# Kernel optimization log

Hardware: AMD Instinct MI355X
Metric: run time of the kernel (lower is better)

The kernel has to match this reference:

```python
import jax, jax.numpy as jnp
import numpy as np

HEADS = 8
HEAD_DIM = 48  # 384 / 8
WINDOW = 64
SCALE = HEAD_DIM ** -0.5


def setup_inputs() -> dict:
    key = jax.random.key(0)
    ks = jax.random.split(key, 8)
    B, T, C, M = 128, 256, 384, 512
    x = jax.random.normal(ks[0], (B, T, C), dtype=jnp.float32)
    mem = jax.random.normal(ks[1], (M, C), dtype=jnp.float32)
    loss_mask = jax.random.uniform(ks[2], (B, T), dtype=jnp.float32)
    # parameters (torch Linear equivalents, stored as [in, out])
    s = 1.0 / np.sqrt(C)
    Wqkv = jax.random.uniform(ks[3], (C, 3 * C), dtype=jnp.float32, minval=-s, maxval=s)
    bqkv = jax.random.uniform(ks[4], (3 * C,), dtype=jnp.float32, minval=-s, maxval=s)
    Wproj = jax.random.uniform(ks[5], (C, C), dtype=jnp.float32, minval=-s, maxval=s)
    bproj = jax.random.uniform(ks[6], (C,), dtype=jnp.float32, minval=-s, maxval=s)
    gate = jnp.ones((C,), dtype=jnp.float32)
    return {"x": x, "mem": mem, "loss_mask": loss_mask, "Wqkv": Wqkv,
            "bqkv": bqkv, "Wproj": Wproj, "bproj": bproj, "gate": gate}


def reference(x, mem, loss_mask, Wqkv, bqkv, Wproj, bproj, gate):
    B, T, C = x.shape
    M = mem.shape[0]
    qkv = x @ Wqkv + bqkv                       # [B, T, 3C]
    q, k, v = jnp.split(qkv, 3, axis=-1)
    # concat raw memory onto keys/values
    m = jnp.broadcast_to(mem[None], (B, M, C))
    k = jnp.concatenate([m, k], axis=1)          # [B, M+T, C]
    v = jnp.concatenate([m, v], axis=1)

    def heads(t):
        return t.reshape(B, -1, HEADS, HEAD_DIM).transpose(0, 2, 1, 3)
    qh, kh, vh = heads(q), heads(k), heads(v)    # [B, H, L, hd]

    att = jnp.einsum('bhqd,bhkd->bhqk', qh, kh) * SCALE  # [B, H, T, M+T]
    # causal + local-window mask on the self (non-mem) key block; mem unmasked
    i = jnp.arange(T)[:, None]
    j = jnp.arange(T)[None, :]
    self_mask = (j <= i) & (jnp.abs(i - j) <= WINDOW)    # [T, T]
    full_mask = jnp.concatenate(
        [jnp.ones((T, M), dtype=bool), self_mask], axis=1)  # [T, M+T]
    att = jnp.where(full_mask[None, None], att, -jnp.inf)
    p = jax.nn.softmax(att, axis=-1)
    y = jnp.einsum('bhqk,bhkd->bhqd', p, vh)     # [B, H, T, hd]
    y = y.transpose(0, 2, 1, 3).reshape(B, T, C)
    out = (y * gate) @ Wproj + bproj
    out = out * loss_mask[..., None]
    return out
```

## Files before the change

### kernel.cpp

```cpp
#include <hip/hip_runtime.h>
#include <hip/hip_bf16.h>

typedef __bf16 bf16_t;
typedef __bf16 bf16x4 __attribute__((ext_vector_type(4)));
typedef __bf16 bf16x8 __attribute__((ext_vector_type(8)));
typedef float f32x4 __attribute__((ext_vector_type(4)));
typedef unsigned int u32;
typedef unsigned int u32x4 __attribute__((ext_vector_type(4)));

struct alignas(16) V16 { unsigned long long x, y; };

#define SC2 0.20823437553929245f
#define NEGBIG -3.0e38f

static __device__ __forceinline__ bf16_t f2b(float f) {
  union { float f; unsigned u; } v; v.f = f;
  unsigned r = v.u + 0x7fffu + ((v.u >> 16) & 1u);
  unsigned short h = (unsigned short)(r >> 16);
  return __builtin_bit_cast(bf16_t, h);
}

static __device__ __forceinline__ f32x4 mfma16(bf16x8 a, bf16x8 b, f32x4 c) {
  return __builtin_amdgcn_mfma_f32_16x16x32_bf16(a, b, c, 0, 0, 0);
}

static __device__ __forceinline__ float exp2f_(float x) {
#if __has_builtin(__builtin_amdgcn_exp2f)
  return __builtin_amdgcn_exp2f(x);
#else
  return __expf(x * 0.6931471805599453f);
#endif
}

static __device__ __forceinline__ u32 cvtpk(float lo, float hi) {
  u32 r;
  asm("v_cvt_pk_bf16_f32 %0, %1, %2" : "=v"(r) : "v"(lo), "v"(hi));
  return r;
}

static __device__ __forceinline__ void gload16(const void* g, void* l) {
  __builtin_amdgcn_global_load_lds(
      (__attribute__((address_space(1))) void*)(unsigned long long)(size_t)g,
      (__attribute__((address_space(3))) void*)(unsigned)(size_t)l,
      16, 0, 0);
}

__global__ void k_xconv(const float* __restrict__ x, bf16_t* __restrict__ xb) {
  size_t i = ((size_t)blockIdx.x * 256 + threadIdx.x) * 8;
  float4 a0 = *(const float4*)(x + i);
  float4 a1 = *(const float4*)(x + i + 4);
  bf16x8 t;
  t[0] = f2b(a0.x); t[1] = f2b(a0.y); t[2] = f2b(a0.z); t[3] = f2b(a0.w);
  t[4] = f2b(a1.x); t[5] = f2b(a1.y); t[6] = f2b(a1.z); t[7] = f2b(a1.w);
  *(bf16x8*)(xb + i) = t;
}

__global__ void k_wprep(const float* __restrict__ W, bf16_t* __restrict__ Wp) {
  int idx = blockIdx.x * 256 + threadIdx.x;
  if (idx >= 1536 * 384) return;
  int c2 = idx / 384, k = idx - c2 * 384;
  int sec = c2 >> 9, within = c2 & 511, hh = within >> 6, d = within & 63;
  float v = (d < 48) ? W[k * 1152 + sec * 384 + hh * 48 + d] : 0.f;
  Wp[idx] = f2b(v);
}

__global__ void k_bprep(const float* __restrict__ bq, float* __restrict__ bp) {
  int c2 = blockIdx.x * 256 + threadIdx.x;
  if (c2 >= 1536) return;
  int sec = c2 >> 9, within = c2 & 511, hh = within >> 6, d = within & 63;
  bp[c2] = (d < 48) ? bq[sec * 384 + hh * 48 + d] : 0.f;
}

template<int K, int N>
__global__ void k_convT(const float* __restrict__ W, bf16_t* __restrict__ Wt) {
  int idx = blockIdx.x * 256 + threadIdx.x;
  if (idx >= K * N) return;
  int n = idx / K, k = idx - n * K;
  Wt[idx] = f2b(W[k * N + n]);
}

__global__ void k_memh(const float* __restrict__ mem, bf16_t* __restrict__ memh) {
  int idx = blockIdx.x * 256 + threadIdx.x;
  int h = idx >> 15;
  int m = (idx >> 6) & 511;
  int d = idx & 63;
  float v = (d < 48) ? mem[m * 384 + h * 48 + d] : 0.f;
  memh[idx] = f2b(v);
}

__global__ void k_memT(const float* __restrict__ mem, bf16_t* __restrict__ memT) {
  int idx = blockIdx.x * 256 + threadIdx.x;
  int h = idx / (48 * 512);
  int r = idx - h * 48 * 512;
  int d = r >> 9;
  int m = r & 511;
  memT[idx] = f2b(mem[m * 384 + h * 48 + d]);
}

__global__ __launch_bounds__(256) void k_gemm_qkv(
    const bf16_t* __restrict__ xb, const bf16_t* __restrict__ Wt,
    const float* __restrict__ biasp,
    bf16_t* __restrict__ qh, bf16_t* __restrict__ kh, bf16_t* __restrict__ vT)
{
  __shared__ __align__(16) char smem[32768];
  const int tid = threadIdx.x;
  const int lane = tid & 63;
  const int j16 = lane & 15;
  const int g = lane >> 4;
  const int wid = tid >> 6;
  const int wr = wid >> 1, wc = wid & 1;
  const int rowBase = blockIdx.x * 128;
  const int colBase = blockIdx.y * 128;
  const int srow = tid >> 2, skc = (tid & 3) * 8;

  f32x4 acc[4][4] = {};

#define STAGE_G(k0, bufidx) do { \
    char* A_ = smem + (bufidx) * 16384; \
    char* B_ = A_ + 8192; \
    gload16(xb + (size_t)(rowBase + srow) * 384 + (k0) + skc, A_ + tid * 16); \
    gload16(xb + (size_t)(rowBase + 64 + srow) * 384 + (k0) + skc, A_ + 4096 + tid * 16); \
    gload16(Wt + (size_t)(colBase + srow) * 384 + (k0) + skc, B_ + tid * 16); \
    gload16(Wt + (size_t)(colBase + 64 + srow) * 384 + (k0) + skc, B_ + 4096 + tid * 16); \
  } while (0)

  STAGE_G(0, 0);
  __syncthreads();
  for (int i = 0; i < 12; ++i) {
    const int cur = i & 1;
    if (i < 11) STAGE_G((i + 1) * 32, cur ^ 1);
    const bf16_t* As = (const bf16_t*)(smem + cur * 16384);
    const bf16_t* Bs = As + 4096;
    bf16x8 af[4], bfr[4];
#pragma unroll
    for (int mb = 0; mb < 4; ++mb)
      af[mb] = *(const bf16x8*)&As[(wr * 64 + mb * 16 + j16) * 32 + g * 8];
#pragma unroll
    for (int nb = 0; nb < 4; ++nb)
      bfr[nb] = *(const bf16x8*)&Bs[(wc * 64 + nb * 16 + j16) * 32 + g * 8];
#pragma unroll
    for (int mb = 0; mb < 4; ++mb)
#pragma unroll
      for (int nb = 0; nb < 4; ++nb)
        acc[mb][nb] = mfma16(af[mb], bfr[nb], acc[mb][nb]);
    __syncthreads();
  }
#undef STAGE_G

  const int sec = colBase >> 9;
  const int b = rowBase >> 8;
  const int tBase = rowBase & 255;
  if (sec < 2) {
    bf16_t* dst0 = (sec == 0) ? qh : kh;
    const int hBase = (colBase - sec * 512) >> 6;
    bf16_t* C = (bf16_t*)smem;
#pragma unroll
    for (int nb = 0; nb < 4; ++nb) {
      const int c_loc = wc * 64 + nb * 16 + j16;
      const float bv = biasp[colBase + c_loc];
#pragma unroll
      for (int mb = 0; mb < 4; ++mb)
#pragma unroll
        for (int r = 0; r < 4; ++r) {
          const int t_loc = wr * 64 + mb * 16 + g * 4 + r;
          C[t_loc * 128 + c_loc] = f2b(acc[mb][nb][r] + bv);
        }
    }
    __syncthreads();
#pragma unroll
    for (int ch = 0; ch < 2; ++ch) {
      const int h = hBase + ch;
      bf16_t* dst = dst0 + (((size_t)(b * 8 + h) * 256 + tBase) << 6);
#pragma unroll
      for (int p = 0; p < 4; ++p) {
        const int k = tid + p * 256;
        const int t_loc = k >> 3;
        V16 v = *(const V16*)&C[t_loc * 128 + ch * 64 + (k & 7) * 8];
        *(V16*)&dst[(size_t)k * 8] = v;
      }
    }
  } else {
#pragma unroll
    for (int nb = 0; nb < 4; ++nb) {
      const int cl = wc * 64 + nb * 16 + j16;
      const int vcol = (colBase - 1024) + cl;
      const int hh = vcol >> 6, d = vcol & 63;
      const float bv = biasp[colBase + cl];
      if (d < 48) {
#pragma unroll
        for (int mb = 0; mb < 4; ++mb) {
          bf16x4 pk;
#pragma unroll
          for (int r = 0; r < 4; ++r) pk[r] = f2b(acc[mb][nb][r] + bv);
          const int t0 = tBase + wr * 64 + mb * 16 + g * 4;
          *(bf16x4*)&vT[((size_t)(b * 8 + hh) * 48 + d) * 256 + t0] = pk;
        }
      }
    }
  }
}

__global__ __launch_bounds__(512, 2) void k_attn(
    const bf16_t* __restrict__ qh, const bf16_t* __restrict__ kh,
    const bf16_t* __restrict__ vT, const bf16_t* __restrict__ memh,
    const bf16_t* __restrict__ memT,
    const float* __restrict__ gate, bf16_t* __restrict__ yp)
{
  __shared__ __align__(16) char smem[57344];
  const int tid = threadIdx.x;
  const int lane = tid & 63;
  const int j16 = lane & 15;
  const int g = lane >> 4;
  const int w = tid >> 6;
  const int qc = blockIdx.x, h = blockIdx.y, b = blockIdx.z;
  const int bh = b * 8 + h;
  const int qw = qc * 128 + w * 16;

  const int key1 = tid >> 3;
  const int doffK = (((tid & 7) << 4) ^ ((key1 & 7) << 4)) >> 1;
  const int dv1 = tid >> 4;
  const int kvV = (((tid & 15) << 4) ^ ((dv1 & 7) << 4)) >> 1;

  bf16x8 qf0, qf1;
  {
    const bf16_t* qp = qh + ((size_t)(bh << 8) + qw + j16) * 64 + g * 8;
    qf0 = *(const bf16x8*)qp;
    qf1 = *(const bf16x8*)(qp + 32);
  }
  float m_r = -1e30f, l_r = 0.f;
  f32x4 o0 = {}, o1 = {}, o2 = {};
  const int nt = (qc == 1) ? 6 : 5;

#define STAGE_A(it_, buf_) do { \
    const bool im_ = (it_) < 4; \
    const int kb_ = im_ ? 0 : ((it_) - 4) * 128; \
    const bf16_t* ks_ = im_ ? memh + ((size_t)h * 512 + (it_) * 128) * 64 \
                            : kh + ((size_t)(bh << 8) + kb_) * 64; \
    const bf16_t* vs_; int vst_, vc_; \
    if (im_) { vs_ = memT + (size_t)h * 48 * 512; vst_ = 512; vc_ = (it_) * 128; } \
    else     { vs_ = vT + (size_t)bh * 48 * 256;  vst_ = 256; vc_ = kb_; } \
    char* K_ = smem + (buf_) * 28672; \
    char* V_ = K_ + 16384; \
    gload16(ks_ + key1 * 64 + doffK,        K_ + tid * 16); \
    gload16(ks_ + (key1 + 64) * 64 + doffK, K_ + 8192 + tid * 16); \
    gload16(vs_ + (size_t)dv1 * vst_ + vc_ + kvV, V_ + tid * 16); \
    if (tid < 256) \
      gload16(vs_ + (size_t)(dv1 + 32) * vst_ + vc_ + kvV, V_ + 8192 + tid * 16); \
  } while (0)

  STAGE_A(0, 0);
  __syncthreads();

  for (int it = 0; it < nt; ++it) {
    const int cur = it & 1;
    if (it + 1 < nt) STAGE_A(it + 1, cur ^ 1);

    const bool isMem = (it < 4);
    const int kb0 = (it - 4) * 128;
    if (isMem || !(kb0 > qw + 15 || kb0 + 127 < qw - 64)) {
      const char* K = smem + cur * 28672;
      const char* V = K + 16384;

      f32x4 s[8];
#pragma unroll
      for (int kb = 0; kb < 8; ++kb) {
        const int key = kb * 16 + j16;
        const int swz = (key & 7) << 4;
        bf16x8 k0v = *(const bf16x8*)(K + ((key * 128 + g * 16) ^ swz));
        bf16x8 k1v = *(const bf16x8*)(K + ((key * 128 + 64 + g * 16) ^ swz));
        f32x4 t4 = {};
        t4 = mfma16(k0v, qf0, t4);
        t4 = mfma16(k1v, qf1, t4);
        s[kb] = t4;
      }

      float mt = NEGBIG;
      if (!isMem) {
#pragma unroll
        for (int kb = 0; kb < 8; ++kb) {
          const int dbase = kb0 + kb * 16 + g * 4 - qw - j16;
#pragma unroll
          for (int r = 0; r < 4; ++r) {
            float sv = s[kb][r] * SC2;
            sv = ((unsigned)(dbase + r + 64) <= 64u) ? sv : NEGBIG;
            s[kb][r] = sv;
            mt = fmaxf(mt, sv);
          }
        }
      } else {
#pragma unroll
        for (int kb = 0; kb < 8; ++kb)
#pragma unroll
          for (int r = 0; r < 4; ++r) {
            float sv = s[kb][r] * SC2;
            s[kb][r] = sv;
            mt = fmaxf(mt, sv);
          }
      }
      mt = fmaxf(mt, __shfl_xor(mt, 16));
      mt = fmaxf(mt, __shfl_xor(mt, 32));

      const float mn = fmaxf(m_r, mt);
      const float alpha = exp2f_(m_r - mn);
      m_r = mn;
      o0 *= alpha; o1 *= alpha; o2 *= alpha;

      float ls = 0.f;
#pragma unroll
      for (int kb = 0; kb < 8; ++kb)
#pragma unroll
        for (int r = 0; r < 4; ++r) {
          float p = exp2f_(s[kb][r] - mn);
          s[kb][r] = p;
          ls += p;
        }
      ls += __shfl_xor(ls, 16);
      ls += __shfl_xor(ls, 32);
      l_r = l_r * alpha + ls;

      u32 pku[16];
#pragma unroll
      for (int kb = 0; kb < 8; ++kb) {
        pku[kb * 2]     = cvtpk(s[kb][0], s[kb][1]);
        pku[kb * 2 + 1] = cvtpk(s[kb][2], s[kb][3]);
      }

#pragma unroll
      for (int kqq = 0; kqq < 4; ++kqq) {
        u32x4 pv = { pku[4 * kqq], pku[4 * kqq + 1], pku[4 * kqq + 2], pku[4 * kqq + 3] };
        bf16x8 pb = __builtin_bit_cast(bf16x8, pv);
#pragma unroll
        for (int db = 0; db < 3; ++db) {
          const int d = db * 16 + j16;
          const int swzd = (d & 7) << 4;
          bf16x4 lo = *(const bf16x4*)(V + ((d * 256 + kqq * 64 + g * 8) ^ swzd));
          bf16x4 hi = *(const bf16x4*)(V + ((d * 256 + kqq * 64 + 32 + g * 8) ^ swzd));
          bf16x8 av = __builtin_shufflevector(lo, hi, 0, 1, 2, 3, 4, 5, 6, 7);
          if (db == 0)      o0 = mfma16(av, pb, o0);
          else if (db == 1) o1 = mfma16(av, pb, o1);
          else              o2 = mfma16(av, pb, o2);
        }
      }
    }
    __syncthreads();
  }
#undef STAGE_A

  const float inv = 1.0f / l_r;
  const int q = qw + j16;
#pragma unroll
  for (int db = 0; db < 3; ++db) {
    f32x4 oo = (db == 0) ? o0 : ((db == 1) ? o1 : o2);
    const int c0 = db * 16 + g * 4;
    bf16x4 pack;
#pragma unroll
    for (int r = 0; r < 4; ++r)
      pack[r] = f2b(oo[r] * inv * gate[h * 48 + c0 + r]);
    *(bf16x4*)(yp + ((size_t)(bh << 8) + q) * 48 + c0) = pack;
  }
}

__global__ __launch_bounds__(256) void k_gemm_proj(
    const bf16_t* __restrict__ yp, const bf16_t* __restrict__ Wt,
    const float* __restrict__ bias, const float* __restrict__ lm,
    float* __restrict__ out)
{
  __shared__ __align__(16) char smem[32768];
  const int tid = threadIdx.x;
  const int lane = tid & 63;
  const int j16 = lane & 15;
  const int g = lane >> 4;
  const int wid = tid >> 6;
  const int wr = wid >> 1, wc = wid & 1;
  const int rowBase = blockIdx.x * 128;
  const int colBase = blockIdx.y * 128;
  const int srow = tid >> 2, skc = (tid & 3) * 8;
  const int bb = rowBase >> 8, tb = rowBase & 255;

  f32x4 acc[4][4] = {};

#define STAGE_P(k0, bufidx) do { \
    char* A_ = smem + (bufidx) * 16384; \
    char* B_ = A_ + 8192; \
    const int c_ = (k0) + skc; \
    const int hh_ = (int)(((unsigned)c_ * 1366u) >> 16); \
    const int d_ = c_ - hh_ * 48; \
    gload16(yp + ((size_t)(bb * 8 + hh_) * 256 + tb + srow) * 48 + d_, A_ + tid * 16); \
    gload16(yp + ((size_t)(bb * 8 + hh_) * 256 + tb + 64 + srow) * 48 + d_, A_ + 4096 + tid * 16); \
    gload16(Wt + (size_t)(colBase + srow) * 384 + (k0) + skc, B_ + tid * 16); \
    gload16(Wt + (size_t)(colBase + 64 + srow) * 384 + (k0) + skc, B_ + 4096 + tid * 16); \
  } while (0)

  STAGE_P(0, 0);
  __syncthreads();
  for (int i = 0; i < 12; ++i) {
    const int cur = i & 1;
    if (i < 11) STAGE_P((i + 1) * 32, cur ^ 1);
    const bf16_t* As = (const bf16_t*)(smem + cur * 16384);
    const bf16_t* Bs = As + 4096;
    bf16x8 af[4], bfr[4];
#pragma unroll
    for (int mb = 0; mb < 4; ++mb)
      af[mb] = *(const bf16x8*)&As[(wr * 64 + mb * 16 + j16) * 32 + g * 8];
#pragma unroll
    for (int nb = 0; nb < 4; ++nb)
      bfr[nb] = *(const bf16x8*)&Bs[(wc * 64 + nb * 16 + j16) * 32 + g * 8];
#pragma unroll
    for (int mb = 0; mb < 4; ++mb)
#pragma unroll
      for (int nb = 0; nb < 4; ++nb)
        acc[mb][nb] = mfma16(af[mb], bfr[nb], acc[mb][nb]);
    __syncthreads();
  }
#undef STAGE_P

#pragma unroll
  for (int nb = 0; nb < 4; ++nb) {
    int col = colBase + wc * 64 + nb * 16 + j16;
    float bv = bias[col];
#pragma unroll
    for (int mb = 0; mb < 4; ++mb) {
#pragma unroll
      for (int r = 0; r < 4; ++r) {
        int row = rowBase + wr * 64 + mb * 16 + g * 4 + r;
        out[(size_t)row * 384 + col] = (acc[mb][nb][r] + bv) * lm[row];
      }
    }
  }
}

extern "C" void kernel_launch(void* const* d_in, const int* in_sizes, int n_in,
                              void* d_out, int out_size, void* d_ws, size_t ws_size,
                              hipStream_t stream) {
  const float* x     = (const float*)d_in[0];
  const float* mem   = (const float*)d_in[1];
  const float* lm    = (const float*)d_in[2];
  const float* Wqkv  = (const float*)d_in[3];
  const float* bqkv  = (const float*)d_in[4];
  const float* Wproj = (const float*)d_in[5];
  const float* bproj = (const float*)d_in[6];
  const float* gate  = (const float*)d_in[7];
  float* out = (float*)d_out;

  char* ws = (char*)d_ws;
  bf16_t* wqkvt = (bf16_t*)ws;  ws += (size_t)1536 * 384 * 2;
  float*  biasp = (float*)ws;   ws += (size_t)1536 * 4;
  bf16_t* wprojt = (bf16_t*)ws; ws += (size_t)384 * 384 * 2;
  bf16_t* memh = (bf16_t*)ws;   ws += (size_t)8 * 512 * 64 * 2;
  bf16_t* memT = (bf16_t*)ws;   ws += (size_t)8 * 48 * 512 * 2;
  bf16_t* qh = (bf16_t*)ws;     ws += (size_t)128 * 8 * 256 * 64 * 2;
  bf16_t* kh = (bf16_t*)ws;     ws += (size_t)128 * 8 * 256 * 64 * 2;
  bf16_t* vT = (bf16_t*)ws;     ws += (size_t)128 * 8 * 48 * 256 * 2;
  bf16_t* xb = (bf16_t*)ws;
  bf16_t* yp = xb;

  k_xconv<<<6144, 256, 0, stream>>>(x, xb);
  k_wprep<<<2304, 256, 0, stream>>>(Wqkv, wqkvt);
  k_bprep<<<6, 256, 0, stream>>>(bqkv, biasp);
  k_convT<384, 384><<<576, 256, 0, stream>>>(Wproj, wprojt);
  k_memh<<<1024, 256, 0, stream>>>(mem, memh);
  k_memT<<<768, 256, 0, stream>>>(mem, memT);
  k_gemm_qkv<<<dim3(256, 12), 256, 0, stream>>>(xb, wqkvt, biasp, qh, kh, vT);
  k_attn<<<dim3(2, 8, 128), 512, 0, stream>>>(qh, kh, vT, memh, memT, gate, yp);
  k_gemm_proj<<<dim3(256, 3), 256, 0, stream>>>(yp, wprojt, bproj, lm, out);
}
```

Measured before the change: 309.3 us.

## Unpad QKV GEMM, fuse prep kernels, merge query chunks in attention block

Combines all weight/memory preparation and q/k padding zeroing into one kernel, removes the padded 64-wide head layout from the QKV weight GEMM so it computes only 1152 columns, and folds the softmax scale into q. The attention kernel now processes both 128-query chunks per (batch, head) in one block, reusing each staged K/V tile for two query groups. This cuts GEMM work, launches and redundant K/V loads, at the cost of fewer attention blocks and higher register pressure.

```diff
diff --git a/kernel.cpp b/kernel.cpp
--- a/kernel.cpp
+++ b/kernel.cpp
@@ -55,51 +55,41 @@
   *(bf16x8*)(xb + i) = t;
 }
 
-__global__ void k_wprep(const float* __restrict__ W, bf16_t* __restrict__ Wp) {
+__global__ void k_prep(const float* __restrict__ Wqkv, const float* __restrict__ Wproj,
+                       const float* __restrict__ mem,
+                       bf16_t* __restrict__ wqkvt, bf16_t* __restrict__ wprojt,
+                       bf16_t* __restrict__ memh, bf16_t* __restrict__ memT,
+                       bf16_t* __restrict__ qh, bf16_t* __restrict__ kh) {
   int idx = blockIdx.x * 256 + threadIdx.x;
-  if (idx >= 1536 * 384) return;
-  int c2 = idx / 384, k = idx - c2 * 384;
-  int sec = c2 >> 9, within = c2 & 511, hh = within >> 6, d = within & 63;
-  float v = (d < 48) ? W[k * 1152 + sec * 384 + hh * 48 + d] : 0.f;
-  Wp[idx] = f2b(v);
-}
-
-__global__ void k_bprep(const float* __restrict__ bq, float* __restrict__ bp) {
-  int c2 = blockIdx.x * 256 + threadIdx.x;
-  if (c2 >= 1536) return;
-  int sec = c2 >> 9, within = c2 & 511, hh = within >> 6, d = within & 63;
-  bp[c2] = (d < 48) ? bq[sec * 384 + hh * 48 + d] : 0.f;
-}
-
-template<int K, int N>
-__global__ void k_convT(const float* __restrict__ W, bf16_t* __restrict__ Wt) {
-  int idx = blockIdx.x * 256 + threadIdx.x;
-  if (idx >= K * N) return;
-  int n = idx / K, k = idx - n * K;
-  Wt[idx] = f2b(W[k * N + n]);
-}
-
-__global__ void k_memh(const float* __restrict__ mem, bf16_t* __restrict__ memh) {
-  int idx = blockIdx.x * 256 + threadIdx.x;
-  int h = idx >> 15;
-  int m = (idx >> 6) & 511;
-  int d = idx & 63;
-  float v = (d < 48) ? mem[m * 384 + h * 48 + d] : 0.f;
-  memh[idx] = f2b(v);
-}
-
-__global__ void k_memT(const float* __restrict__ mem, bf16_t* __restrict__ memT) {
-  int idx = blockIdx.x * 256 + threadIdx.x;
-  int h = idx / (48 * 512);
-  int r = idx - h * 48 * 512;
-  int d = r >> 9;
-  int m = r & 511;
-  memT[idx] = f2b(mem[m * 384 + h * 48 + d]);
+  if (idx < 442368) {
+    int n = idx / 384, k = idx - n * 384;
+    wqkvt[idx] = f2b(Wqkv[k * 1152 + n]);
+  } else if ((idx -= 442368) < 147456) {
+    int n = idx / 384, k = idx - n * 384;
+    wprojt[idx] = f2b(Wproj[k * 384 + n]);
+  } else if ((idx -= 147456) < 262144) {
+    int h = idx >> 15, m = (idx >> 6) & 511, d = idx & 63;
+    memh[idx] = f2b(d < 48 ? mem[m * 384 + h * 48 + d] : 0.f);
+  } else if ((idx -= 262144) < 196608) {
+    int h = idx / 24576;
+    int r = idx - h * 24576;
+    int d = r >> 9, m = r & 511;
+    memT[idx] = f2b(mem[m * 384 + h * 48 + d]);
+  } else if ((idx -= 196608) < 524288) {
+    int row = idx >> 1, half = idx & 1;
+    V16 z; z.x = 0; z.y = 0;
+    *(V16*)((char*)qh + (size_t)row * 128 + 96 + half * 16) = z;
+  } else {
+    idx -= 524288;
+    int row = idx >> 1, half = idx & 1;
+    V16 z; z.x = 0; z.y = 0;
+    *(V16*)((char*)kh + (size_t)row * 128 + 96 + half * 16) = z;
+  }
 }
 
 __global__ __launch_bounds__(256) void k_gemm_qkv(
     const bf16_t* __restrict__ xb, const bf16_t* __restrict__ Wt,
-    const float* __restrict__ biasp,
+    const float* __restrict__ bias,
     bf16_t* __restrict__ qh, bf16_t* __restrict__ kh, bf16_t* __restrict__ vT)
 {
   __shared__ __align__(16) char smem[32768];
@@ -110,7 +100,9 @@
   const int wid = tid >> 6;
   const int wr = wid >> 1, wc = wid & 1;
   const int rowBase = blockIdx.x * 128;
-  const int colBase = blockIdx.y * 128;
+  const int by = blockIdx.y;
+  const int colBase = by * 128;
+  const int sec = by / 3;
   const int srow = tid >> 2, skc = (tid & 3) * 8;
 
   f32x4 acc[4][4] = {};
@@ -147,54 +139,51 @@
   }
 #undef STAGE_G
 
-  const int sec = colBase >> 9;
   const int b = rowBase >> 8;
   const int tBase = rowBase & 255;
   if (sec < 2) {
     bf16_t* dst0 = (sec == 0) ? qh : kh;
-    const int hBase = (colBase - sec * 512) >> 6;
+    const float scl = (sec == 0) ? SC2 : 1.0f;
+    const int colSec = colBase - sec * 384;
     bf16_t* C = (bf16_t*)smem;
 #pragma unroll
     for (int nb = 0; nb < 4; ++nb) {
       const int c_loc = wc * 64 + nb * 16 + j16;
-      const float bv = biasp[colBase + c_loc];
+      const float bv = bias[colBase + c_loc];
 #pragma unroll
       for (int mb = 0; mb < 4; ++mb)
 #pragma unroll
         for (int r = 0; r < 4; ++r) {
           const int t_loc = wr * 64 + mb * 16 + g * 4 + r;
-          C[t_loc * 128 + c_loc] = f2b(acc[mb][nb][r] + bv);
+          C[t_loc * 128 + c_loc] = f2b((acc[mb][nb][r] + bv) * scl);
         }
     }
     __syncthreads();
 #pragma unroll
-    for (int ch = 0; ch < 2; ++ch) {
-      const int h = hBase + ch;
-      bf16_t* dst = dst0 + (((size_t)(b * 8 + h) * 256 + tBase) << 6);
-#pragma unroll
-      for (int p = 0; p < 4; ++p) {
-        const int k = tid + p * 256;
-        const int t_loc = k >> 3;
-        V16 v = *(const V16*)&C[t_loc * 128 + ch * 64 + (k & 7) * 8];
-        *(V16*)&dst[(size_t)k * 8] = v;
-      }
+    for (int p = 0; p < 8; ++p) {
+      const int k = tid + p * 256;
+      const int t_loc = k >> 4;
+      const int col = colSec + (k & 15) * 8;
+      const int h = (int)(((unsigned)col * 1366u) >> 16);
+      const int d0 = col - h * 48;
+      V16 v = *(const V16*)&C[t_loc * 128 + (k & 15) * 8];
+      *(V16*)&dst0[(((size_t)(b * 8 + h) * 256 + tBase + t_loc) << 6) + d0] = v;
     }
   } else {
 #pragma unroll
     for (int nb = 0; nb < 4; ++nb) {
       const int cl = wc * 64 + nb * 16 + j16;
-      const int vcol = (colBase - 1024) + cl;
-      const int hh = vcol >> 6, d = vcol & 63;
-      const float bv = biasp[colBase + cl];
-      if (d < 48) {
-#pragma unroll
-        for (int mb = 0; mb < 4; ++mb) {
-          bf16x4 pk;
-#pragma unroll
-          for (int r = 0; r < 4; ++r) pk[r] = f2b(acc[mb][nb][r] + bv);
-          const int t0 = tBase + wr * 64 + mb * 16 + g * 4;
-          *(bf16x4*)&vT[((size_t)(b * 8 + hh) * 48 + d) * 256 + t0] = pk;
-        }
+      const int vcol = (colBase - 768) + cl;
+      const int hh = (int)(((unsigned)vcol * 1366u) >> 16);
+      const int d = vcol - hh * 48;
+      const float bv = bias[colBase + cl];
+#pragma unroll
+      for (int mb = 0; mb < 4; ++mb) {
+        bf16x4 pk;
+#pragma unroll
+        for (int r = 0; r < 4; ++r) pk[r] = f2b(acc[mb][nb][r] + bv);
+        const int t0 = tBase + wr * 64 + mb * 16 + g * 4;
+        *(bf16x4*)&vT[((size_t)(b * 8 + hh) * 48 + d) * 256 + t0] = pk;
       }
     }
   }
@@ -212,24 +201,23 @@
   const int j16 = lane & 15;
   const int g = lane >> 4;
   const int w = tid >> 6;
-  const int qc = blockIdx.x, h = blockIdx.y, b = blockIdx.z;
+  const int h = blockIdx.x, b = blockIdx.y;
   const int bh = b * 8 + h;
-  const int qw = qc * 128 + w * 16;
 
   const int key1 = tid >> 3;
   const int doffK = (((tid & 7) << 4) ^ ((key1 & 7) << 4)) >> 1;
   const int dv1 = tid >> 4;
   const int kvV = (((tid & 15) << 4) ^ ((dv1 & 7) << 4)) >> 1;
 
-  bf16x8 qf0, qf1;
-  {
-    const bf16_t* qp = qh + ((size_t)(bh << 8) + qw + j16) * 64 + g * 8;
-    qf0 = *(const bf16x8*)qp;
-    qf1 = *(const bf16x8*)(qp + 32);
-  }
-  float m_r = -1e30f, l_r = 0.f;
-  f32x4 o0 = {}, o1 = {}, o2 = {};
-  const int nt = (qc == 1) ? 6 : 5;
+  bf16x8 qfa[2], qfb[2];
+#pragma unroll
+  for (int qg = 0; qg < 2; ++qg) {
+    const bf16_t* qp = qh + ((size_t)(bh << 8) + qg * 128 + w * 16 + j16) * 64 + g * 8;
+    qfa[qg] = *(const bf16x8*)qp;
+    qfb[qg] = *(const bf16x8*)(qp + 32);
+  }
+  float m_r[2] = {-1e30f, -1e30f}, l_r[2] = {0.f, 0.f};
+  f32x4 o[2][3] = {};
 
 #define STAGE_A(it_, buf_) do { \
     const bool im_ = (it_) < 4; \
@@ -251,15 +239,19 @@
   STAGE_A(0, 0);
   __syncthreads();
 
-  for (int it = 0; it < nt; ++it) {
+  for (int it = 0; it < 6; ++it) {
     const int cur = it & 1;
-    if (it + 1 < nt) STAGE_A(it + 1, cur ^ 1);
+    if (it < 5) STAGE_A(it + 1, cur ^ 1);
 
     const bool isMem = (it < 4);
     const int kb0 = (it - 4) * 128;
-    if (isMem || !(kb0 > qw + 15 || kb0 + 127 < qw - 64)) {
-      const char* K = smem + cur * 28672;
-      const char* V = K + 16384;
+    const char* K = smem + cur * 28672;
+    const char* V = K + 16384;
+
+#pragma unroll
+    for (int qg = 0; qg < 2; ++qg) {
+      const int qw = qg * 128 + w * 16;
+      if (!isMem && (kb0 > qw + 15 || kb0 + 127 < qw - 64)) continue;
 
       f32x4 s[8];
 #pragma unroll
@@ -269,41 +261,37 @@
         bf16x8 k0v = *(const bf16x8*)(K + ((key * 128 + g * 16) ^ swz));
         bf16x8 k1v = *(const bf16x8*)(K + ((key * 128 + 64 + g * 16) ^ swz));
         f32x4 t4 = {};
-        t4 = mfma16(k0v, qf0, t4);
-        t4 = mfma16(k1v, qf1, t4);
+        t4 = mfma16(k0v, qfa[qg], t4);
+        t4 = mfma16(k1v, qfb[qg], t4);
         s[kb] = t4;
       }
 
-      float mt = NEGBIG;
       if (!isMem) {
 #pragma unroll
         for (int kb = 0; kb < 8; ++kb) {
           const int dbase = kb0 + kb * 16 + g * 4 - qw - j16;
 #pragma unroll
-          for (int r = 0; r < 4; ++r) {
-            float sv = s[kb][r] * SC2;
-            sv = ((unsigned)(dbase + r + 64) <= 64u) ? sv : NEGBIG;
-            s[kb][r] = sv;
-            mt = fmaxf(mt, sv);
-          }
+          for (int r = 0; r < 4; ++r)
+            s[kb][r] = ((unsigned)(dbase + r + 64) <= 64u) ? s[kb][r] : NEGBIG;
         }
-      } else {
-#pragma unroll
-        for (int kb = 0; kb < 8; ++kb)
-#pragma unroll
-          for (int r = 0; r < 4; ++r) {
-            float sv = s[kb][r] * SC2;
-            s[kb][r] = sv;
-            mt = fmaxf(mt, sv);
-          }
-      }
+      }
+      f32x4 mv = s[0];
+#pragma unroll
+      for (int kb = 1; kb < 8; ++kb) {
+        mv[0] = fmaxf(mv[0], s[kb][0]);
+        mv[1] = fmaxf(mv[1], s[kb][1]);
+        mv[2] = fmaxf(mv[2], s[kb][2]);
+        mv[3] = fmaxf(mv[3], s[kb][3]);
+      }
+      float mt = fmaxf(fmaxf(mv[0], mv[1]), fmaxf(mv[2], mv[3]));
       mt = fmaxf(mt, __shfl_xor(mt, 16));
       mt = fmaxf(mt, __shfl_xor(mt, 32));
 
-      const float mn = fmaxf(m_r, mt);
-      const float alpha = exp2f_(m_r - mn);
-      m_r = mn;
-      o0 *= alpha; o1 *= alpha; o2 *= alpha;
+      const float mn = fmaxf(m_r[qg], mt);
+      const float alpha = exp2f_(m_r[qg] - mn);
+      m_r[qg] = mn;
+#pragma unroll
+      for (int db = 0; db < 3; ++db) o[qg][db] *= alpha;
 
       float ls = 0.f;
 #pragma unroll
@@ -316,7 +304,7 @@
         }
       ls += __shfl_xor(ls, 16);
       ls += __shfl_xor(ls, 32);
-      l_r = l_r * alpha + ls;
+      l_r[qg] = l_r[qg] * alpha + ls;
 
       u32 pku[16];
 #pragma unroll
@@ -336,9 +324,7 @@
           bf16x4 lo = *(const bf16x4*)(V + ((d * 256 + kqq * 64 + g * 8) ^ swzd));
           bf16x4 hi = *(const bf16x4*)(V + ((d * 256 + kqq * 64 + 32 + g * 8) ^ swzd));
           bf16x8 av = __builtin_shufflevector(lo, hi, 0, 1, 2, 3, 4, 5, 6, 7);
-          if (db == 0)      o0 = mfma16(av, pb, o0);
-          else if (db == 1) o1 = mfma16(av, pb, o1);
-          else              o2 = mfma16(av, pb, o2);
+          o[qg][db] = mfma16(av, pb, o[qg][db]);
         }
       }
     }
@@ -346,17 +332,19 @@
   }
 #undef STAGE_A
 
-  const float inv = 1.0f / l_r;
-  const int q = qw + j16;
-#pragma unroll
-  for (int db = 0; db < 3; ++db) {
-    f32x4 oo = (db == 0) ? o0 : ((db == 1) ? o1 : o2);
-    const int c0 = db * 16 + g * 4;
-    bf16x4 pack;
-#pragma unroll
-    for (int r = 0; r < 4; ++r)
-      pack[r] = f2b(oo[r] * inv * gate[h * 48 + c0 + r]);
-    *(bf16x4*)(yp + ((size_t)(bh << 8) + q) * 48 + c0) = pack;
+#pragma unroll
+  for (int qg = 0; qg < 2; ++qg) {
+    const float inv = 1.0f / l_r[qg];
+    const int q = qg * 128 + w * 16 + j16;
+#pragma unroll
+    for (int db = 0; db < 3; ++db) {
+      const int c0 = db * 16 + g * 4;
+      bf16x4 pack;
+#pragma unroll
+      for (int r = 0; r < 4; ++r)
+        pack[r] = f2b(o[qg][db][r] * inv * gate[h * 48 + c0 + r]);
+      *(bf16x4*)(yp + ((size_t)(bh << 8) + q) * 48 + c0) = pack;
+    }
   }
 }
 
@@ -443,8 +431,7 @@
   float* out = (float*)d_out;
 
   char* ws = (char*)d_ws;
-  bf16_t* wqkvt = (bf16_t*)ws;  ws += (size_t)1536 * 384 * 2;
-  float*  biasp = (float*)ws;   ws += (size_t)1536 * 4;
+  bf16_t* wqkvt = (bf16_t*)ws;  ws += (size_t)1152 * 384 * 2;
   bf16_t* wprojt = (bf16_t*)ws; ws += (size_t)384 * 384 * 2;
   bf16_t* memh = (bf16_t*)ws;   ws += (size_t)8 * 512 * 64 * 2;
   bf16_t* memT = (bf16_t*)ws;   ws += (size_t)8 * 48 * 512 * 2;
@@ -455,12 +442,8 @@
   bf16_t* yp = xb;
 
   k_xconv<<<6144, 256, 0, stream>>>(x, xb);
-  k_wprep<<<2304, 256, 0, stream>>>(Wqkv, wqkvt);
-  k_bprep<<<6, 256, 0, stream>>>(bqkv, biasp);
-  k_convT<384, 384><<<576, 256, 0, stream>>>(Wproj, wprojt);
-  k_memh<<<1024, 256, 0, stream>>>(mem, memh);
-  k_memT<<<768, 256, 0, stream>>>(mem, memT);
-  k_gemm_qkv<<<dim3(256, 12), 256, 0, stream>>>(xb, wqkvt, biasp, qh, kh, vT);
-  k_attn<<<dim3(2, 8, 128), 512, 0, stream>>>(qh, kh, vT, memh, memT, gate, yp);
+  k_prep<<<8192, 256, 0, stream>>>(Wqkv, Wproj, mem, wqkvt, wprojt, memh, memT, qh, kh);
+  k_gemm_qkv<<<dim3(256, 9), 256, 0, stream>>>(xb, wqkvt, bqkv, qh, kh, vT);
+  k_attn<<<dim3(8, 128), 512, 0, stream>>>(qh, kh, vT, memh, memT, gate, yp);
   k_gemm_proj<<<dim3(256, 3), 256, 0, stream>>>(yp, wprojt, bproj, lm, out);
 }
```

After: 276.6 us. 1.12x faster.
